# Optimization experiments

Measured on AMD Instinct MI355X. Metric: run time of the kernel, lower is better.

The kernel has to match this reference:

```python
import jax, jax.numpy as jnp
import numpy as np

N_EMBD = 1024
HEAD_SIZE = 128

def setup_inputs() -> dict:
    key = jax.random.key(0)
    k1, k2, k3, k4 = jax.random.split(key, 4)
    x = jax.random.normal(k1, (8, 2048, N_EMBD), dtype=jnp.float32)
    # Linear(n_embd, head_size, bias=False): y = x @ W, W: [n_embd, head_size]
    s = 1.0 / np.sqrt(N_EMBD)
    Wk = jax.random.uniform(k2, (N_EMBD, HEAD_SIZE), jnp.float32, -s, s)
    Wq = jax.random.uniform(k3, (N_EMBD, HEAD_SIZE), jnp.float32, -s, s)
    Wv = jax.random.uniform(k4, (N_EMBD, HEAD_SIZE), jnp.float32, -s, s)
    return {"x": x, "Wk": Wk, "Wq": Wq, "Wv": Wv}

def reference(x, Wk, Wq, Wv):
    B, T, C = x.shape
    H = Wk.shape[1]
    k = jnp.einsum('btc,ch->bth', x, Wk)
    q = jnp.einsum('btc,ch->bth', x, Wq)
    v = jnp.einsum('btc,ch->bth', x, Wv)
    # scores [B, T, T], causal mask, scaled by head_size**-0.5
    wei = jnp.einsum('bqh,bkh->bqk', q, k) * (H ** -0.5)
    causal = jnp.tril(jnp.ones((T, T), dtype=bool))
    wei = jnp.where(causal, wei, -jnp.inf)
    wei = jax.nn.softmax(wei, axis=-1)
    # dropout p=0.0 (eval mode): identity
    out = jnp.einsum('bqk,bkh->bqh', wei, v)
    return out
```

## Files before the change

kernel.cpp:

```cpp
#include <hip/hip_runtime.h>
#include <hip/hip_bf16.h>
#include <stdint.h>

typedef short v8s __attribute__((ext_vector_type(8)));
typedef float v4f __attribute__((ext_vector_type(4)));
typedef float v16f __attribute__((ext_vector_type(16)));

#define N_EMBD 1024
#define HEAD 128
#define TOKENS 16384
#define T_SEQ 2048
#define BATCH 8
#define BPB 96

__device__ __forceinline__ short f2bf(float f) {
    union { float f; uint32_t u; } c; c.f = f;
    uint32_t u = c.u;
    uint32_t r = (u + 0x7fffu + ((u >> 16) & 1u)) >> 16;
    return (short)r;
}

__device__ __forceinline__ float bf2f(short s) {
    union { uint32_t u; float f; } c; c.u = ((uint32_t)(uint16_t)s) << 16;
    return c.f;
}

__global__ __launch_bounds__(256)
void wt_kernel(const float* __restrict__ Wq, const float* __restrict__ Wk,
               const float* __restrict__ Wv, short* __restrict__ wt) {
    int tid = blockIdx.x * 256 + threadIdx.x;
    int w   = tid >> 17;
    int rem = tid & 131071;
    int c = rem >> 7, h = rem & 127;
    const float* src = (w == 0) ? Wq : ((w == 1) ? Wk : Wv);
    wt[w * 131072 + h * 1024 + c] = f2bf(src[rem]);
}

__global__ __launch_bounds__(256)
void qkv_gemm(const float* __restrict__ x, const short* __restrict__ wt,
              short* __restrict__ qkv, short* __restrict__ vT) {
    const int bid = blockIdx.x;
    const int xcd = bid & 7, q = bid >> 3;
    const int mt  = xcd * 32 + q / 3;
    const int w   = q % 3;
    const int m0  = mt * 64;

    __shared__ short smem[2][64 * 40 + 128 * 40];

    const int t = threadIdx.x;
    const int lane = t & 63, wv = t >> 6;
    const int l31 = lane & 31, l1 = lane >> 5;
    const int wm = wv & 1, wn = wv >> 1;

    const short* wtw = wt + w * 131072;

    const int arow = t >> 3, ac4 = t & 7;
    const int brow = t >> 2, bc8 = t & 3;
    const float* aptr0 = x + (size_t)(m0 + arow) * 1024 + ac4 * 4;
    const float* aptr1 = x + (size_t)(m0 + arow + 32) * 1024 + ac4 * 4;
    const short* bptr0 = wtw + brow * 1024 + bc8 * 8;
    const short* bptr1 = wtw + (brow + 64) * 1024 + bc8 * 8;

    float4 a00 = *(const float4*)(aptr0);
    float4 a01 = *(const float4*)(aptr1);
    uint4  b00 = *(const uint4*)(bptr0);
    uint4  b01 = *(const uint4*)(bptr1);
    float4 a10 = *(const float4*)(aptr0 + 32);
    float4 a11 = *(const float4*)(aptr1 + 32);
    uint4  b10 = *(const uint4*)(bptr0 + 32);
    uint4  b11 = *(const uint4*)(bptr1 + 32);

    v16f acc[2];
    for (int i = 0; i < 16; ++i) { acc[0][i] = 0.f; acc[1][i] = 0.f; }

#define STAGE(BUF, A0, A1, B0, B1) do {                                          \
        short* sA_ = smem[BUF]; short* sB_ = smem[BUF] + 64 * 40;                \
        union { short s[4]; uint64_t u; } p0_, p1_;                              \
        p0_.s[0] = f2bf((A0).x); p0_.s[1] = f2bf((A0).y);                        \
        p0_.s[2] = f2bf((A0).z); p0_.s[3] = f2bf((A0).w);                        \
        p1_.s[0] = f2bf((A1).x); p1_.s[1] = f2bf((A1).y);                        \
        p1_.s[2] = f2bf((A1).z); p1_.s[3] = f2bf((A1).w);                        \
        *(uint64_t*)(&sA_[arow * 40 + ac4 * 4]) = p0_.u;                         \
        *(uint64_t*)(&sA_[(arow + 32) * 40 + ac4 * 4]) = p1_.u;                  \
        *(uint4*)(&sB_[brow * 40 + bc8 * 8]) = (B0);                             \
        *(uint4*)(&sB_[(brow + 64) * 40 + bc8 * 8]) = (B1);                      \
    } while (0)

#define COMPUTE(BUF) do {                                                        \
        const short* sA_ = smem[BUF];                                            \
        const short* sB_ = smem[BUF] + 64 * 40;                                  \
        for (int ks = 0; ks < 2; ++ks) {                                         \
            v8s a_ = *(const v8s*)&sA_[(wm * 32 + l31) * 40 + ks * 16 + l1 * 8]; \
            v8s b0_ = *(const v8s*)&sB_[(wn * 64 + l31) * 40 + ks * 16 + l1 * 8];\
            acc[0] = __builtin_amdgcn_mfma_f32_32x32x16_bf16(a_, b0_, acc[0], 0, 0, 0); \
            v8s b1_ = *(const v8s*)&sB_[(wn * 64 + 32 + l31) * 40 + ks * 16 + l1 * 8]; \
            acc[1] = __builtin_amdgcn_mfma_f32_32x32x16_bf16(a_, b1_, acc[1], 0, 0, 0); \
        }                                                                        \
    } while (0)

    STAGE(0, a00, a01, b00, b01);

    for (int it = 0; it < 32; it += 2) {
        if (it + 2 < 32) {
            int kk = (it + 2) * 32;
            a00 = *(const float4*)(aptr0 + kk);
            a01 = *(const float4*)(aptr1 + kk);
            b00 = *(const uint4*)(bptr0 + kk);
            b01 = *(const uint4*)(bptr1 + kk);
        }
        __syncthreads();
        COMPUTE(0);
        STAGE(1, a10, a11, b10, b11);
        if (it + 3 < 32) {
            int kk = (it + 3) * 32;
            a10 = *(const float4*)(aptr0 + kk);
            a11 = *(const float4*)(aptr1 + kk);
            b10 = *(const uint4*)(bptr0 + kk);
            b11 = *(const uint4*)(bptr1 + kk);
        }
        __syncthreads();
        COMPUTE(1);
        if (it + 2 < 32) STAGE(0, a00, a01, b00, b01);
    }

#undef STAGE
#undef COMPUTE

    if (w < 2) {
        short* outw = qkv + (size_t)w * TOKENS * HEAD;
        for (int ni = 0; ni < 2; ++ni) {
            int col = wn * 64 + ni * 32 + l31;
            for (int reg = 0; reg < 16; ++reg) {
                int m = (reg & 3) + 8 * (reg >> 2) + 4 * l1;
                outw[(size_t)(m0 + wm * 32 + m) * HEAD + col] = f2bf(acc[ni][reg]);
            }
        }
    } else {
        __syncthreads();
        short* sT = (short*)smem;
        for (int ni = 0; ni < 2; ++ni) {
            int col = wn * 64 + ni * 32 + l31;
            for (int g = 0; g < 4; ++g) {
                union { short s[4]; uint64_t u; } pk;
                for (int r = 0; r < 4; ++r) pk.s[r] = f2bf(acc[ni][g * 4 + r]);
                *(uint64_t*)(&sT[col * 72 + wm * 32 + 8 * g + 4 * l1]) = pk.u;
            }
        }
        __syncthreads();
        for (int it = 0; it < 4; ++it) {
            int c = it * 256 + t;
            int col = c >> 3, c8 = c & 7;
            uint4 d = *(const uint4*)(&sT[col * 72 + c8 * 8]);
            *(uint4*)(&vT[(size_t)col * TOKENS + m0 + c8 * 8]) = d;
        }
    }
}

__global__ __launch_bounds__(256)
void attn_kernel(const short* __restrict__ qb, const short* __restrict__ kb,
                 const short* __restrict__ vT, short* __restrict__ po,
                 float* __restrict__ pl) {
    const int bid = blockIdx.x;
    const int b  = bid & 7;
    const int r0 = bid >> 3;
    int qt2 = 0, c0 = 0;
    for (;;) { int sz = (2 * qt2 + 4) / 3; if (r0 < c0 + sz) break; c0 += sz; ++qt2; }
    const int s = r0 - c0;
    const int q0 = qt2 * 128;
    const int nkt = 2 * qt2 + 2;
    const int kt0 = s * 3;
    const int kt1 = (kt0 + 3 < nkt) ? (kt0 + 3) : nkt;

    __shared__ short sK[64 * 128];
    __shared__ short sV[128 * 64];
    __shared__ short sP[128 * 72];

    const int t = threadIdx.x;
    const int wv = t >> 6, lane = t & 63, ln = lane & 15, qd = lane >> 4;
    const int wrow0 = q0 + wv * 32;

    v8s qf[2][4];
    for (int qg = 0; qg < 2; ++qg) {
        const short* qrow = qb + ((size_t)(b * T_SEQ + wrow0 + qg * 16 + ln)) * HEAD;
        for (int ks = 0; ks < 4; ++ks)
            qf[qg][ks] = *(const v8s*)(qrow + ks * 32 + qd * 8);
    }

    v4f o[2][8] = {};
    float rs[2] = {0.f, 0.f};
    const float sc = 1.4426950408889634f / 11.313708498984761f;

    for (int kt = kt0; kt < kt1; ++kt) {
        __syncthreads();
        const short* kbase = kb + ((size_t)(b * T_SEQ + kt * 64)) * HEAD;
        for (int it = 0; it < 4; ++it) {
            int c = it * 256 + t;
            int row = c >> 4, ch = c & 15;
            uint4 d = *(const uint4*)(kbase + row * HEAD + ch * 8);
            int sch = (ch & 8) | ((ch ^ row) & 7);
            *(uint4*)(&sK[row * 128 + sch * 8]) = d;
        }
        const short* vbase = vT + (size_t)(b * T_SEQ + kt * 64);
        for (int it = 0; it < 4; ++it) {
            int c = it * 256 + t;
            int dd = c >> 3, ch = c & 7;
            uint4 d = *(const uint4*)(vbase + (size_t)dd * TOKENS + ch * 8);
            *(uint4*)(&sV[dd * 64 + ((ch ^ dd) & 7) * 8]) = d;
        }
        __syncthreads();

        if (kt * 64 >= wrow0 + 32) continue;

        v4f st[2][4] = {};
        for (int ni = 0; ni < 4; ++ni) {
            int krow = ni * 16 + ln;
            for (int ks = 0; ks < 4; ++ks) {
                int ch = ks * 4 + qd;
                v8s kf = *(const v8s*)&sK[krow * 128 + ((ch & 8) | ((ch ^ krow) & 7)) * 8];
                st[0][ni] = __builtin_amdgcn_mfma_f32_16x16x32_bf16(kf, qf[0][ks], st[0][ni], 0, 0, 0);
                st[1][ni] = __builtin_amdgcn_mfma_f32_16x16x32_bf16(kf, qf[1][ks], st[1][ni], 0, 0, 0);
            }
        }

        const bool needMask = (kt * 64 + 63 > wrow0);
        for (int qg = 0; qg < 2; ++qg) {
            int prow = wv * 32 + qg * 16 + ln;
            int qrow_g = wrow0 + qg * 16 + ln;
            for (int ni = 0; ni < 4; ++ni) {
                union { short s[4]; uint64_t u; } pk;
                for (int r = 0; r < 4; ++r) {
                    float p = exp2f(st[qg][ni][r] * sc);
                    int kg = kt * 64 + ni * 16 + qd * 4 + r;
                    if (needMask && kg > qrow_g) p = 0.f;
                    rs[qg] += p;
                    pk.s[r] = f2bf(p);
                }
                *(uint64_t*)(&sP[prow * 72 + ni * 16 + qd * 4]) = pk.u;
            }
        }

        for (int kk2 = 0; kk2 < 2; ++kk2) {
            v8s pf0 = *(const v8s*)&sP[(wv * 32 + ln) * 72 + kk2 * 32 + qd * 8];
            v8s pf1 = *(const v8s*)&sP[(wv * 32 + 16 + ln) * 72 + kk2 * 32 + qd * 8];
            for (int oni = 0; oni < 8; ++oni) {
                int dd = oni * 16 + ln;
                int ch = kk2 * 4 + qd;
                v8s vf = *(const v8s*)&sV[dd * 64 + ((ch ^ dd) & 7) * 8];
                o[0][oni] = __builtin_amdgcn_mfma_f32_16x16x32_bf16(vf, pf0, o[0][oni], 0, 0, 0);
                o[1][oni] = __builtin_amdgcn_mfma_f32_16x16x32_bf16(vf, pf1, o[1][oni], 0, 0, 0);
            }
        }
    }

    float lsum[2];
    for (int qg = 0; qg < 2; ++qg) {
        float v = rs[qg];
        v += __shfl_xor(v, 16);
        v += __shfl_xor(v, 32);
        lsum[qg] = v;
    }

    short* pob = po + (size_t)bid * 128 * 128;
    for (int qg = 0; qg < 2; ++qg)
        for (int oni = 0; oni < 8; ++oni) {
            union { short s[4]; uint2 u; } pk;
            for (int r = 0; r < 4; ++r) pk.s[r] = f2bf(o[qg][oni][r]);
            *(uint2*)(&pob[(((qg * 8 + oni) * 4 + wv) * 64 + lane) * 4]) = pk.u;
        }
    if (lane < 16)
        for (int qg = 0; qg < 2; ++qg)
            pl[bid * 128 + wv * 32 + qg * 16 + lane] = lsum[qg];
}

__global__ __launch_bounds__(256)
void combine_kernel(const short* __restrict__ po, const float* __restrict__ pl,
                    float* __restrict__ out) {
    const int bid = blockIdx.x;
    const int dh  = bid & 1;
    const int qh  = (bid >> 1) & 1;
    const int qt2 = (bid >> 2) & 15;
    const int b   = bid >> 6;
    int cum = 0;
    for (int j = 0; j < qt2; ++j) cum += (2 * j + 4) / 3;
    const int S = (2 * qt2 + 4) / 3;

    const int t = threadIdx.x;
    const int wv = t >> 6, lane = t & 63, ln = lane & 15, qd = lane >> 4;

    float l = 0.f;
    float accv[4][4] = {};

    for (int si = 0; si < S; ++si) {
        int slot = (cum + si) * 8 + b;
        l += pl[slot * 128 + wv * 32 + qh * 16 + ln];
        const short* pob = po + (size_t)slot * 16384;
        for (int oi = 0; oi < 4; ++oi) {
            int oni = dh * 4 + oi;
            union { short s[4]; uint2 u; } pk;
            pk.u = *(const uint2*)(&pob[(((qh * 8 + oni) * 4 + wv) * 64 + lane) * 4]);
            for (int r = 0; r < 4; ++r) accv[oi][r] += bf2f(pk.s[r]);
        }
    }
    float inv = 1.f / l;
    float* ob = out + ((size_t)(b * T_SEQ) + qt2 * 128 + wv * 32 + qh * 16 + ln) * HEAD;
    for (int oi = 0; oi < 4; ++oi) {
        float4 o4 = make_float4(accv[oi][0] * inv, accv[oi][1] * inv,
                                accv[oi][2] * inv, accv[oi][3] * inv);
        *(float4*)(ob + (dh * 4 + oi) * 16 + qd * 4) = o4;
    }
}

extern "C" void kernel_launch(void* const* d_in, const int* in_sizes, int n_in,
                              void* d_out, int out_size, void* d_ws, size_t ws_size,
                              hipStream_t stream) {
    const float* x  = (const float*)d_in[0];
    const float* Wk = (const float*)d_in[1];
    const float* Wq = (const float*)d_in[2];
    const float* Wv = (const float*)d_in[3];
    float* out = (float*)d_out;

    char* ws = (char*)d_ws;
    short* wt = (short*)ws;
    short* qb = (short*)(ws + 0x100000u);
    short* kb = (short*)(ws + 0x500000u);
    short* vT = (short*)(ws + 0x900000u);
    short* po = (short*)(ws + 0xD00000u);
    float* pl = (float*)(ws + 0x2500000u);
    short* qkv = qb;

    wt_kernel<<<1536, 256, 0, stream>>>(Wq, Wk, Wv, wt);
    qkv_gemm<<<768, 256, 0, stream>>>(x, wt, qkv, vT);
    attn_kernel<<<BATCH * BPB, 256, 0, stream>>>(qb, kb, vT, po, pl);
    combine_kernel<<<512, 256, 0, stream>>>(po, pl, out);
}
```

Measured before the change: 168.2 us.

## Register-prefetch next K/V tile in attention and use lighter LDS-only barriers

The attention loop now loads the next K and V tile from global memory into registers while the current tile is being computed, then writes them to shared memory at the top of the next iteration. This hides global load latency behind the MFMA work. It also replaces __syncthreads with a custom barrier that waits only on LDS counters (lgkmcnt) rather than on all outstanding memory operations, so in-flight global prefetches are not drained at each barrier, in both the projection GEMM and the attention kernel. The cost is more registers per thread, which may lower occupancy, and reliance on hand-written inline asm for barrier correctness.

```diff
diff --git a/kernel.cpp b/kernel.cpp
--- a/kernel.cpp
+++ b/kernel.cpp
@@ -12,6 +12,8 @@
 #define T_SEQ 2048
 #define BATCH 8
 #define BPB 96
+
+#define BAR() asm volatile("s_waitcnt lgkmcnt(0)\n\ts_barrier" ::: "memory")
 
 __device__ __forceinline__ short f2bf(float f) {
     union { float f; uint32_t u; } c; c.f = f;
@@ -108,7 +110,7 @@
             b00 = *(const uint4*)(bptr0 + kk);
             b01 = *(const uint4*)(bptr1 + kk);
         }
-        __syncthreads();
+        BAR();
         COMPUTE(0);
         STAGE(1, a10, a11, b10, b11);
         if (it + 3 < 32) {
@@ -118,7 +120,7 @@
             b10 = *(const uint4*)(bptr0 + kk);
             b11 = *(const uint4*)(bptr1 + kk);
         }
-        __syncthreads();
+        BAR();
         COMPUTE(1);
         if (it + 2 < 32) STAGE(0, a00, a01, b00, b01);
     }
@@ -190,24 +192,39 @@
     float rs[2] = {0.f, 0.f};
     const float sc = 1.4426950408889634f / 11.313708498984761f;
 
+    const int krow_s = t >> 4, kch_s = t & 15;
+    const int vdd_s  = t >> 3, vch_s = t & 7;
+
+    uint4 kreg[4], vreg[4];
+    {
+        const short* kb0 = kb + ((size_t)(b * T_SEQ + kt0 * 64)) * HEAD;
+        const short* vb0 = vT + (size_t)(b * T_SEQ + kt0 * 64);
+        for (int it = 0; it < 4; ++it)
+            kreg[it] = *(const uint4*)(kb0 + (it * 16 + krow_s) * HEAD + kch_s * 8);
+        for (int it = 0; it < 4; ++it)
+            vreg[it] = *(const uint4*)(vb0 + (size_t)(it * 32 + vdd_s) * TOKENS + vch_s * 8);
+    }
+
     for (int kt = kt0; kt < kt1; ++kt) {
-        __syncthreads();
-        const short* kbase = kb + ((size_t)(b * T_SEQ + kt * 64)) * HEAD;
+        BAR();
         for (int it = 0; it < 4; ++it) {
-            int c = it * 256 + t;
-            int row = c >> 4, ch = c & 15;
-            uint4 d = *(const uint4*)(kbase + row * HEAD + ch * 8);
+            int row = it * 16 + krow_s, ch = kch_s;
             int sch = (ch & 8) | ((ch ^ row) & 7);
-            *(uint4*)(&sK[row * 128 + sch * 8]) = d;
-        }
-        const short* vbase = vT + (size_t)(b * T_SEQ + kt * 64);
+            *(uint4*)(&sK[row * 128 + sch * 8]) = kreg[it];
+        }
         for (int it = 0; it < 4; ++it) {
-            int c = it * 256 + t;
-            int dd = c >> 3, ch = c & 7;
-            uint4 d = *(const uint4*)(vbase + (size_t)dd * TOKENS + ch * 8);
-            *(uint4*)(&sV[dd * 64 + ((ch ^ dd) & 7) * 8]) = d;
-        }
-        __syncthreads();
+            int dd = it * 32 + vdd_s;
+            *(uint4*)(&sV[dd * 64 + ((vch_s ^ dd) & 7) * 8]) = vreg[it];
+        }
+        if (kt + 1 < kt1) {
+            const short* kb1 = kb + ((size_t)(b * T_SEQ + (kt + 1) * 64)) * HEAD;
+            const short* vb1 = vT + (size_t)(b * T_SEQ + (kt + 1) * 64);
+            for (int it = 0; it < 4; ++it)
+                kreg[it] = *(const uint4*)(kb1 + (it * 16 + krow_s) * HEAD + kch_s * 8);
+            for (int it = 0; it < 4; ++it)
+                vreg[it] = *(const uint4*)(vb1 + (size_t)(it * 32 + vdd_s) * TOKENS + vch_s * 8);
+        }
+        BAR();
 
         if (kt * 64 >= wrow0 + 32) continue;
 
```

Measured after the change: 184.8 us. +9.9%, slower.
